# Optimization experiments

Hardware: AMD Instinct MI355X
Metric: run time of the kernel (lower is better)

## Reference

```python
import jax, jax.numpy as jnp
import numpy as np


def setup_inputs() -> dict:
    key = jax.random.key(0)
    ks = jax.random.split(key, 7)
    H, O, B, T = 256, 128, 2048, 100
    s = 1.0 / np.sqrt(H)
    return {
        "C": jax.random.normal(ks[0], (B, H), dtype=jnp.float32),
        "W_ih": jax.random.uniform(ks[1], (4 * H, H), jnp.float32, -s, s),
        "W_hh": jax.random.uniform(ks[2], (4 * H, H), jnp.float32, -s, s),
        "b_ih": jax.random.uniform(ks[3], (4 * H,), jnp.float32, -s, s),
        "b_hh": jax.random.uniform(ks[4], (4 * H,), jnp.float32, -s, s),
        "W_out": jax.random.uniform(ks[5], (O, H), jnp.float32, -s, s),
        "b_out": jax.random.uniform(ks[6], (O,), jnp.float32, -s, s),
        "max_seq_len": T,
    }


def reference(C, W_ih, W_hh, b_ih, b_hh, W_out, b_out, max_seq_len):
    B, H = C.shape
    # Input contribution is the same at every step (the module re-feeds C).
    x_gates = C @ W_ih.T + b_ih + b_hh  # [B, 4H]

    def step(carry, _):
        h, c = carry
        gates = x_gates + h @ W_hh.T  # [B, 4H]
        i, f, g, o = jnp.split(gates, 4, axis=-1)  # torch gate order: i,f,g,o
        c_new = jax.nn.sigmoid(f) * c + jax.nn.sigmoid(i) * jnp.tanh(g)
        h_new = jax.nn.sigmoid(o) * jnp.tanh(c_new)
        y = h_new @ W_out.T + b_out  # [B, O]
        return (h_new, c_new), y

    init = (jnp.zeros((B, H), C.dtype), jnp.zeros((B, H), C.dtype))
    _, ys = jax.lax.scan(step, init, None, length=max_seq_len)
    return ys  # [T, B, O]
```

## Files before the change

### kernel.cpp

```cpp
#include <hip/hip_runtime.h>
#include <hip/hip_bf16.h>

typedef __attribute__((ext_vector_type(8))) short  bf16x8;
typedef __attribute__((ext_vector_type(4))) short  s16x4;
typedef __attribute__((ext_vector_type(4))) float  f32x4;

#define LOG2E 1.44269504088896340736f
template<int N> struct ic { static constexpr int v = N; };

__device__ __forceinline__ unsigned short f2bf(float x) {
    union { float f; unsigned int u; } v; v.f = x;
    unsigned int u = v.u;
    u += 0x7fffu + ((u >> 16) & 1u);
    return (unsigned short)(u >> 16);
}
__device__ __forceinline__ float fast_sigmoid(float x) {
    float e = __builtin_amdgcn_exp2f(-LOG2E * x);
    return __builtin_amdgcn_rcpf(1.0f + e);
}
__device__ __forceinline__ float fast_tanh(float x) {
    float e = __builtin_amdgcn_exp2f(2.0f * LOG2E * x);
    return 1.0f - 2.0f * __builtin_amdgcn_rcpf(1.0f + e);
}

__global__ void pack_w_big(const float* __restrict__ W, unsigned short* __restrict__ dst) {
    int idx  = blockIdx.x * 256 + threadIdx.x;
    int lane = idx & 63;
    int fid  = idx >> 6;
    int j    = fid & 7;
    int kk   = (fid >> 3) & 7;
    int w    = fid >> 6;
    int g    = j >> 1, tn = j & 1;
    int R    = g * 256 + w * 32 + tn * 16 + (lane & 15);
    int kb   = kk * 32 + 4 * (lane >> 4);
    const float* src = W + (size_t)R * 256 + kb;
    union { unsigned short s[8]; uint4 v; } u;
#pragma unroll
    for (int e = 0; e < 8; ++e) {
        int k = (e & 3) + 16 * (e >> 2);
        u.s[e] = f2bf(src[k]);
    }
    *(uint4*)(dst + (size_t)idx * 8) = u.v;
}

__global__ void pack_w_out(const float* __restrict__ W, unsigned short* __restrict__ dst) {
    int idx  = blockIdx.x * 256 + threadIdx.x;
    int lane = idx & 63;
    int fid  = idx >> 6;
    int kk   = fid & 7;
    int wv   = fid >> 3;
    int R    = wv * 16 + (lane & 15);
    int kb   = kk * 32 + 4 * (lane >> 4);
    const float* src = W + (size_t)R * 256 + kb;
    union { unsigned short s[8]; uint4 v; } u;
#pragma unroll
    for (int e = 0; e < 8; ++e) {
        int k = (e & 3) + 16 * (e >> 2);
        u.s[e] = f2bf(src[k]);
    }
    *(uint4*)(dst + (size_t)idx * 8) = u.v;
}

__global__ __launch_bounds__(512) __attribute__((amdgpu_waves_per_eu(2, 2)))
void lstm_gates(const float* __restrict__ C,
                const unsigned short* __restrict__ Wih_p,
                const unsigned short* __restrict__ Whh_p,
                const float* __restrict__ b_ih,
                const float* __restrict__ b_hh,
                unsigned short* __restrict__ H,
                int T, int Btot)
{
    __shared__ short hbuf[2][4096];
    __shared__ short park[8][8][512];
    __shared__ short ring[8][8][512];

    const int tid  = threadIdx.x;
    const int l    = tid & 63;
    const int wid  = tid >> 6;
    const int l15  = l & 15;
    const int g4   = l >> 4;
    const int row0 = blockIdx.x * 16;

    const unsigned short* wib = Wih_p + (size_t)wid * 32768;
    const unsigned short* whb = Whh_p + (size_t)wid * 32768;

    {
        int r  = tid >> 5;
        int cb = tid & 31;
        const float* src = C + (size_t)(row0 + r) * 256 + cb * 8;
        float4 f0 = *(const float4*)(src);
        float4 f1 = *(const float4*)(src + 4);
        int m  = 9 * (r & 7);
        int s0 = cb * 2;
        short* hb = hbuf[0] + r * 256;
        union { unsigned short s[4]; unsigned long long v; } p0, p1;
        p0.s[0] = f2bf(f0.x); p0.s[1] = f2bf(f0.y); p0.s[2] = f2bf(f0.z); p0.s[3] = f2bf(f0.w);
        p1.s[0] = f2bf(f1.x); p1.s[1] = f2bf(f1.y); p1.s[2] = f2bf(f1.z); p1.s[3] = f2bf(f1.w);
        *(unsigned long long*)(hb + ((s0 ^ m) * 4))       = p0.v;
        *(unsigned long long*)(hb + (((s0 + 1) ^ m) * 4)) = p1.v;
    }

    auto issue = [&](short (*dst)[512], int kk, int j) {
        const unsigned short* src = whb + (((size_t)kk * 8 + j) * 64 + l) * 8;
        __builtin_amdgcn_global_load_lds(
            (const __attribute__((address_space(1))) void*)src,
            (__attribute__((address_space(3))) void*)&dst[j][0], 16, 0, 0);
    };
#pragma unroll
    for (int j = 0; j < 8; ++j) issue(park[wid], 4, j);
#pragma unroll
    for (int j = 0; j < 8; ++j) issue(ring[wid], 5, j);

    const int msw = 9 * (l15 & 7);
    auto loadA = [&](const short* buf, int kk) -> bf16x8 {
        int slo = kk * 8 + g4;
        const short* base = buf + l15 * 256;
        s16x4 lo = *(const s16x4*)(base + ((slo ^ msw) * 4));
        s16x4 hi = *(const s16x4*)(base + (((slo + 4) ^ msw) * 4));
        bf16x8 a;
        a[0] = lo[0]; a[1] = lo[1]; a[2] = lo[2]; a[3] = lo[3];
        a[4] = hi[0]; a[5] = hi[1]; a[6] = hi[2]; a[7] = hi[3];
        return a;
    };
    auto loadB = [&](const unsigned short* wb, int kk, int j) -> bf16x8 {
        return *(const bf16x8*)(wb + (((size_t)kk * 8 + j) * 64 + l) * 8);
    };

    __syncthreads();

    f32x4 acc[8];
#pragma unroll
    for (int j = 0; j < 8; ++j) acc[j] = (f32x4){0.f, 0.f, 0.f, 0.f};
#pragma unroll
    for (int kk = 0; kk < 8; ++kk) {
        bf16x8 a = loadA(hbuf[0], kk);
#pragma unroll
        for (int j = 0; j < 8; ++j)
            acc[j] = __builtin_amdgcn_mfma_f32_16x16x32_bf16(a, loadB(wib, kk, j), acc[j], 0, 0, 0);
    }
#pragma unroll
    for (int j = 0; j < 8; ++j) {
        int g = j >> 1, tn = j & 1;
        int col = g * 256 + wid * 32 + tn * 16 + l15;
        float bias = b_ih[col] + b_hh[col];
        acc[j] = acc[j] + bias;
    }
    unsigned xgp[16];
#pragma unroll
    for (int j = 0; j < 8; ++j) {
        xgp[2 * j]     = (unsigned)f2bf(acc[j][0]) | ((unsigned)f2bf(acc[j][1]) << 16);
        xgp[2 * j + 1] = (unsigned)f2bf(acc[j][2]) | ((unsigned)f2bf(acc[j][3]) << 16);
    }
    auto xgu = [&](int j) -> f32x4 {
        union { unsigned u; float f; } c0, c1, c2, c3;
        unsigned u0 = xgp[2 * j], u1 = xgp[2 * j + 1];
        c0.u = u0 << 16; c1.u = u0 & 0xffff0000u;
        c2.u = u1 << 16; c3.u = u1 & 0xffff0000u;
        return (f32x4){c0.f, c1.f, c2.f, c3.f};
    };

    bf16x8 whr[4][8];
#pragma unroll
    for (int kk = 0; kk < 4; ++kk)
#pragma unroll
        for (int j = 0; j < 8; ++j) whr[kk][j] = loadB(whb, kk, j);

    float cst[8];
#pragma unroll
    for (int i = 0; i < 8; ++i) cst[i] = 0.f;

    auto update_write = [&](short* nxtb, unsigned short* hst) {
#pragma unroll
        for (int tn = 0; tn < 2; ++tn) {
#pragma unroll
            for (int rr = 0; rr < 4; ++rr) {
                float iv = fast_sigmoid(acc[0 + tn][rr]);
                float fv = fast_sigmoid(acc[2 + tn][rr]);
                float gv = fast_tanh(acc[4 + tn][rr]);
                float ov = fast_sigmoid(acc[6 + tn][rr]);
                float cn = fv * cst[tn * 4 + rr] + iv * gv;
                cst[tn * 4 + rr] = cn;
                float hn = ov * fast_tanh(cn);
                unsigned short hb = f2bf(hn);
                int row = 4 * g4 + rr;
                int col = wid * 32 + tn * 16 + l15;
                int ps  = (col >> 2) ^ (9 * (row & 7));
                nxtb[row * 256 + ps * 4 + (col & 3)] = (short)hb;
                hst[(size_t)row * 256 + col] = hb;
            }
        }
    };

    update_write(hbuf[1], H + (size_t)row0 * 256);
    __syncthreads();

    auto phaseR0 = [&](const short* curb) {
        bf16x8 a = loadA(curb, 0);
#pragma unroll
        for (int j = 0; j < 8; ++j)
            acc[j] = __builtin_amdgcn_mfma_f32_16x16x32_bf16(a, whr[0][j], xgu(j), 0, 0, 0);
    };
    auto phaseR = [&](auto KK, const short* curb) {
        constexpr int kk = decltype(KK)::v;
        bf16x8 a = loadA(curb, kk);
#pragma unroll
        for (int j = 0; j < 8; ++j)
            acc[j] = __builtin_amdgcn_mfma_f32_16x16x32_bf16(a, whr[kk][j], acc[j], 0, 0, 0);
    };
    auto phaseP = [&](const short* curb) {
        bf16x8 a = loadA(curb, 4);
#pragma unroll
        for (int j = 0; j < 8; ++j) {
            bf16x8 b = *(const bf16x8*)&park[wid][j][l * 8];
            acc[j] = __builtin_amdgcn_mfma_f32_16x16x32_bf16(a, b, acc[j], 0, 0, 0);
        }
    };
    auto phaseS = [&](auto KK, auto NX, const short* curb) {
        constexpr int kk = decltype(KK)::v;
        constexpr int nx = decltype(NX)::v;
        bf16x8 a = loadA(curb, kk);
        asm volatile("s_waitcnt vmcnt(4)" ::: "memory");
#pragma unroll
        for (int j = 0; j < 4; ++j) {
            bf16x8 b = *(const bf16x8*)&ring[wid][j][l * 8];
            acc[j] = __builtin_amdgcn_mfma_f32_16x16x32_bf16(a, b, acc[j], 0, 0, 0);
        }
#pragma unroll
        for (int j = 0; j < 4; ++j) issue(ring[wid], nx, j);
        asm volatile("s_waitcnt vmcnt(4)" ::: "memory");
#pragma unroll
        for (int j = 4; j < 8; ++j) {
            bf16x8 b = *(const bf16x8*)&ring[wid][j][l * 8];
            acc[j] = __builtin_amdgcn_mfma_f32_16x16x32_bf16(a, b, acc[j], 0, 0, 0);
        }
#pragma unroll
        for (int j = 4; j < 8; ++j) issue(ring[wid], nx, j);
    };

    for (int t = 2; t <= T; ++t) {
        const short* curb = hbuf[(t - 1) & 1];
        short*       nxtb = hbuf[t & 1];

        phaseR0(curb);
        phaseR(ic<1>{}, curb);
        phaseR(ic<2>{}, curb);
        phaseR(ic<3>{}, curb);
        phaseP(curb);
        phaseS(ic<5>{}, ic<6>{}, curb);
        phaseS(ic<6>{}, ic<7>{}, curb);
        phaseS(ic<7>{}, ic<5>{}, curb);

        update_write(nxtb, H + ((size_t)(t - 1) * Btot + row0) * 256);

        asm volatile("s_waitcnt lgkmcnt(0)" ::: "memory");
        __builtin_amdgcn_sched_barrier(0);
        __builtin_amdgcn_s_barrier();
    }
}

__global__ __launch_bounds__(512) void out_gemm(
    const unsigned short* __restrict__ Wout_p,
    const float* __restrict__ b_out,
    float* __restrict__ Y)
{
    const int tid = threadIdx.x;
    const int l   = tid & 63;
    const int w   = tid >> 6;
    const int l15 = l & 15;
    const int g4  = l >> 4;
    const size_t rw0 = (size_t)blockIdx.x * 256 + w * 32;
    const unsigned short* Hp = (const unsigned short*)Y;

    bf16x8 a[2][8];
#pragma unroll
    for (int rt = 0; rt < 2; ++rt)
#pragma unroll
        for (int kk = 0; kk < 8; ++kk) {
            const unsigned short* src = Hp + (rw0 + rt * 16 + l15) * 256 + kk * 32 + 4 * g4;
            s16x4 lo = *(const s16x4*)(src);
            s16x4 hi = *(const s16x4*)(src + 16);
            bf16x8 v;
            v[0] = lo[0]; v[1] = lo[1]; v[2] = lo[2]; v[3] = lo[3];
            v[4] = hi[0]; v[5] = hi[1]; v[6] = hi[2]; v[7] = hi[3];
            a[rt][kk] = v;
        }

    f32x4 acc[2][8];
#pragma unroll
    for (int rt = 0; rt < 2; ++rt)
#pragma unroll
        for (int wv = 0; wv < 8; ++wv) acc[rt][wv] = (f32x4){0.f, 0.f, 0.f, 0.f};

#pragma unroll
    for (int kk = 0; kk < 8; ++kk)
#pragma unroll
        for (int wv = 0; wv < 8; ++wv) {
            bf16x8 wf = *(const bf16x8*)(Wout_p + ((size_t)(wv * 8 + kk) * 64 + l) * 8);
            acc[0][wv] = __builtin_amdgcn_mfma_f32_16x16x32_bf16(a[0][kk], wf, acc[0][wv], 0, 0, 0);
            acc[1][wv] = __builtin_amdgcn_mfma_f32_16x16x32_bf16(a[1][kk], wf, acc[1][wv], 0, 0, 0);
        }

#pragma unroll
    for (int wv = 0; wv < 8; ++wv) {
        float by = b_out[wv * 16 + l15];
#pragma unroll
        for (int rt = 0; rt < 2; ++rt)
#pragma unroll
            for (int i = 0; i < 4; ++i)
                Y[(rw0 + rt * 16 + 4 * g4 + i) * 128 + wv * 16 + l15] = acc[rt][wv][i] + by;
    }
}

extern "C" void kernel_launch(void* const* d_in, const int* in_sizes, int n_in,
                              void* d_out, int out_size, void* d_ws, size_t ws_size,
                              hipStream_t stream) {
    const float* C     = (const float*)d_in[0];
    const float* W_ih  = (const float*)d_in[1];
    const float* W_hh  = (const float*)d_in[2];
    const float* b_ih  = (const float*)d_in[3];
    const float* b_hh  = (const float*)d_in[4];
    const float* W_out = (const float*)d_in[5];
    const float* b_out = (const float*)d_in[6];

    const int H    = 256;
    const int Btot = in_sizes[0] / H;
    const int O    = in_sizes[5] / H;
    const int T    = out_size / (Btot * O);

    unsigned short* Whh_p  = (unsigned short*)d_ws;
    unsigned short* Wih_p  = Whh_p + (1 << 18);
    unsigned short* Wout_p = Wih_p + (1 << 18);

    hipLaunchKernelGGL(pack_w_big, dim3(128), dim3(256), 0, stream, W_hh, Whh_p);
    hipLaunchKernelGGL(pack_w_big, dim3(128), dim3(256), 0, stream, W_ih, Wih_p);
    hipLaunchKernelGGL(pack_w_out, dim3(16),  dim3(256), 0, stream, W_out, Wout_p);
    hipLaunchKernelGGL(lstm_gates, dim3(Btot / 16), dim3(512), 0, stream,
                       C, Wih_p, Whh_p, b_ih, b_hh,
                       (unsigned short*)d_out, T, Btot);
    hipLaunchKernelGGL(out_gemm, dim3((T * Btot) / 256), dim3(512), 0, stream,
                       Wout_p, b_out, (float*)d_out);
}
```

Baseline: 653.4 us.

## Replicate streamed W_hh slices per block group to spread global reads

Adds a kernel that copies the streamed part of packed W_hh (k-chunks 5-7) into up to 128 compact copies in workspace. Each recurrent block then streams its ring buffer from the copy chosen by blockIdx modulo the copy count, instead of all blocks reading one shared region. The aim is to spread the per-step global/L2 traffic over more memory channels and cut contention on hot lines. The cost is an extra replication launch that writes several MB. The fallback path when workspace is small reuses the original packed layout with the new compact indexing, which looks inconsistent.

New measurement: 975.4 us. 49.3% more time.

```diff
diff --git a/kernel.cpp b/kernel.cpp
--- a/kernel.cpp
+++ b/kernel.cpp
@@ -61,14 +61,30 @@
     *(uint4*)(dst + (size_t)idx * 8) = u.v;
 }
 
+__global__ void replicate_stream(const unsigned short* __restrict__ Whh_p,
+                                 unsigned short* __restrict__ rep) {
+    int gidx = blockIdx.x * 256 + threadIdx.x;
+    int q    = gidx % 12288;
+    int c    = gidx / 12288;
+    int lane = q & 63;
+    int f    = q >> 6;
+    int j    = f & 7;
+    int kkp  = (f >> 3) % 3;
+    int w    = f / 24;
+    const uint4* src = (const uint4*)(Whh_p + (((size_t)w * 64 + (5 + kkp) * 8 + j) * 64 + lane) * 8);
+    uint4* dst = (uint4*)(rep + (size_t)c * 98304 + ((size_t)q) * 8);
+    *dst = *src;
+}
+
 __global__ __launch_bounds__(512) __attribute__((amdgpu_waves_per_eu(2, 2)))
 void lstm_gates(const float* __restrict__ C,
                 const unsigned short* __restrict__ Wih_p,
                 const unsigned short* __restrict__ Whh_p,
+                const unsigned short* __restrict__ rep,
                 const float* __restrict__ b_ih,
                 const float* __restrict__ b_hh,
                 unsigned short* __restrict__ H,
-                int T, int Btot)
+                int T, int Btot, int ncopies)
 {
     __shared__ short hbuf[2][4096];
     __shared__ short park[8][8][512];
@@ -83,6 +99,8 @@
 
     const unsigned short* wib = Wih_p + (size_t)wid * 32768;
     const unsigned short* whb = Whh_p + (size_t)wid * 32768;
+    const unsigned short* wstr = rep + (size_t)(blockIdx.x % ncopies) * 98304
+                                     + (size_t)wid * 12288;
 
     {
         int r  = tid >> 5;
@@ -100,16 +118,22 @@
         *(unsigned long long*)(hb + (((s0 + 1) ^ m) * 4)) = p1.v;
     }
 
-    auto issue = [&](short (*dst)[512], int kk, int j) {
-        const unsigned short* src = whb + (((size_t)kk * 8 + j) * 64 + l) * 8;
+    auto issueP = [&](int j) {
+        const unsigned short* src = whb + (((size_t)4 * 8 + j) * 64 + l) * 8;
         __builtin_amdgcn_global_load_lds(
             (const __attribute__((address_space(1))) void*)src,
-            (__attribute__((address_space(3))) void*)&dst[j][0], 16, 0, 0);
-    };
-#pragma unroll
-    for (int j = 0; j < 8; ++j) issue(park[wid], 4, j);
-#pragma unroll
-    for (int j = 0; j < 8; ++j) issue(ring[wid], 5, j);
+            (__attribute__((address_space(3))) void*)&park[wid][j][0], 16, 0, 0);
+    };
+    auto issueS = [&](int kkp, int j) {
+        const unsigned short* src = wstr + ((size_t)(kkp * 8 + j) * 64 + l) * 8;
+        __builtin_amdgcn_global_load_lds(
+            (const __attribute__((address_space(1))) void*)src,
+            (__attribute__((address_space(3))) void*)&ring[wid][j][0], 16, 0, 0);
+    };
+#pragma unroll
+    for (int j = 0; j < 8; ++j) issueP(j);
+#pragma unroll
+    for (int j = 0; j < 8; ++j) issueS(0, j);
 
     const int msw = 9 * (l15 & 7);
     auto loadA = [&](const short* buf, int kk) -> bf16x8 {
@@ -215,9 +239,9 @@
             acc[j] = __builtin_amdgcn_mfma_f32_16x16x32_bf16(a, b, acc[j], 0, 0, 0);
         }
     };
-    auto phaseS = [&](auto KK, auto NX, const short* curb) {
-        constexpr int kk = decltype(KK)::v;
-        constexpr int nx = decltype(NX)::v;
+    auto phaseS = [&](auto KK, auto NXP, const short* curb) {
+        constexpr int kk  = decltype(KK)::v;
+        constexpr int nxp = decltype(NXP)::v;
         bf16x8 a = loadA(curb, kk);
         asm volatile("s_waitcnt vmcnt(4)" ::: "memory");
 #pragma unroll
@@ -226,7 +250,7 @@
             acc[j] = __builtin_amdgcn_mfma_f32_16x16x32_bf16(a, b, acc[j], 0, 0, 0);
         }
 #pragma unroll
-        for (int j = 0; j < 4; ++j) issue(ring[wid], nx, j);
+        for (int j = 0; j < 4; ++j) issueS(nxp, j);
         asm volatile("s_waitcnt vmcnt(4)" ::: "memory");
 #pragma unroll
         for (int j = 4; j < 8; ++j) {
@@ -234,7 +258,7 @@
             acc[j] = __builtin_amdgcn_mfma_f32_16x16x32_bf16(a, b, acc[j], 0, 0, 0);
         }
 #pragma unroll
-        for (int j = 4; j < 8; ++j) issue(ring[wid], nx, j);
+        for (int j = 4; j < 8; ++j) issueS(nxp, j);
     };
 
     for (int t = 2; t <= T; ++t) {
@@ -246,9 +270,9 @@
         phaseR(ic<2>{}, curb);
         phaseR(ic<3>{}, curb);
         phaseP(curb);
-        phaseS(ic<5>{}, ic<6>{}, curb);
-        phaseS(ic<6>{}, ic<7>{}, curb);
-        phaseS(ic<7>{}, ic<5>{}, curb);
+        phaseS(ic<5>{}, ic<1>{}, curb);
+        phaseS(ic<6>{}, ic<2>{}, curb);
+        phaseS(ic<7>{}, ic<0>{}, curb);
 
         update_write(nxtb, H + ((size_t)(t - 1) * Btot + row0) * 256);
 
@@ -327,16 +351,34 @@
     const int O    = in_sizes[5] / H;
     const int T    = out_size / (Btot * O);
 
-    unsigned short* Whh_p  = (unsigned short*)d_ws;
-    unsigned short* Wih_p  = Whh_p + (1 << 18);
-    unsigned short* Wout_p = Wih_p + (1 << 18);
+    char* ws = (char*)d_ws;
+    unsigned short* Whh_p  = (unsigned short*)(ws);
+    unsigned short* Wih_p  = (unsigned short*)(ws + (512 << 10));
+    unsigned short* Wout_p = (unsigned short*)(ws + (1024 << 10));
+    unsigned short* rep    = (unsigned short*)(ws + (1088 << 10));
+
+    const size_t copy_bytes = 196608;
+    size_t avail = (ws_size > (1088u << 10)) ? ws_size - (1088u << 10) : 0;
+    int ncopies = (int)(avail / copy_bytes);
+    if (ncopies > 128) ncopies = 128;
+    if (ncopies < 1)   ncopies = 1;
+    bool use_rep = ncopies >= 1 && avail >= copy_bytes;
 
     hipLaunchKernelGGL(pack_w_big, dim3(128), dim3(256), 0, stream, W_hh, Whh_p);
     hipLaunchKernelGGL(pack_w_big, dim3(128), dim3(256), 0, stream, W_ih, Wih_p);
     hipLaunchKernelGGL(pack_w_out, dim3(16),  dim3(256), 0, stream, W_out, Wout_p);
+    if (use_rep) {
+        hipLaunchKernelGGL(replicate_stream, dim3(ncopies * 48), dim3(256), 0, stream,
+                           Whh_p, rep);
+    } else {
+        rep = Whh_p;
+    }
+    if (!use_rep) {
+        ncopies = 1;
+    }
     hipLaunchKernelGGL(lstm_gates, dim3(Btot / 16), dim3(512), 0, stream,
-                       C, Wih_p, Whh_p, b_ih, b_hh,
-                       (unsigned short*)d_out, T, Btot);
+                       C, Wih_p, Whh_p, rep, b_ih, b_hh,
+                       (unsigned short*)d_out, T, Btot, ncopies);
     hipLaunchKernelGGL(out_gemm, dim3((T * Btot) / 256), dim3(512), 0, stream,
                        Wout_p, b_out, (float*)d_out);
 }
```
